# Performance work log

Measured on AMD Instinct MI355X. Metric: run time of the kernel, lower is better.

## Reference

```python
import jax, jax.numpy as jnp
import numpy as np

D_MODEL = 128
N_HEADS = 8
N_POINTS = 8
MAX_RES = 10.0


def setup_inputs() -> dict:
    key = jax.random.key(0)
    ks = jax.random.split(key, 12)
    B, C, H, W = 4, D_MODEL, 128, 128
    nh, P = N_HEADS, N_POINTS
    inp = {
        'nbr_fea': jax.random.normal(ks[0], (B, C, H, W), jnp.float32),
        'ext_fea': jax.random.normal(ks[1], (B, C, H, W), jnp.float32),
        'flow': jax.random.normal(ks[2], (B, 2, H, W), jnp.float32) * 2.0,
        'W_off': jax.random.normal(ks[3], (C, nh * P * 2), jnp.float32) * 0.02,
        'b_off': jax.random.normal(ks[4], (nh * P * 2,), jnp.float32) * 0.02,
        'W_attn': jax.random.normal(ks[5], (C, nh * P), jnp.float32) * 0.02,
        'b_attn': jnp.zeros((nh * P,), jnp.float32),
        'W_val': jax.random.normal(ks[6], (C, C), jnp.float32) * (1.0 / np.sqrt(C)),
        'b_val': jnp.zeros((C,), jnp.float32),
        'W_out': jax.random.normal(ks[7], (C, C), jnp.float32) * (1.0 / np.sqrt(C)),
        'b_out': jnp.zeros((C,), jnp.float32),
    }
    return inp


def _bilinear_gather(value, loc, H, W):
    # value: (B, nh, HW, dh)  loc: (B, nh, Q, P, 2) normalized to [0,1]
    # grid_sample semantics: align_corners=False, zero padding
    B, nh, HW, dh = value.shape
    Q, P = loc.shape[2], loc.shape[3]
    x = loc[..., 0] * W - 0.5  # (B,nh,Q,P) pixel coords
    y = loc[..., 1] * H - 0.5
    x0 = jnp.floor(x)
    y0 = jnp.floor(y)
    wx = x - x0
    wy = y - y0
    out = jnp.zeros((B, nh, Q * P, dh), value.dtype)
    for dx, dy, wgt in ((0, 0, (1 - wx) * (1 - wy)), (1, 0, wx * (1 - wy)),
                        (0, 1, (1 - wx) * wy), (1, 1, wx * wy)):
        xi = x0 + dx
        yi = y0 + dy
        valid = (xi >= 0) & (xi < W) & (yi >= 0) & (yi < H)
        xi_c = jnp.clip(xi, 0, W - 1).astype(jnp.int32)
        yi_c = jnp.clip(yi, 0, H - 1).astype(jnp.int32)
        idx = (yi_c * W + xi_c).reshape(B, nh, Q * P, 1)
        g = jnp.take_along_axis(value, idx, axis=2)  # (B,nh,QP,dh)
        w_eff = (wgt * valid.astype(value.dtype)).reshape(B, nh, Q * P, 1)
        out = out + g * w_eff
    return out.reshape(B, nh, Q, P, dh)


def reference(nbr_fea, ext_fea, flow, W_off, b_off, W_attn, b_attn, W_val, b_val, W_out, b_out):
    B, C, H, W = nbr_fea.shape
    nh, P = N_HEADS, N_POINTS
    dh = C // nh
    Q = H * W
    # normalized reference points (pixel centers / extent)
    ys = (jnp.arange(H, dtype=jnp.float32) + 0.5) / H
    xs = (jnp.arange(W, dtype=jnp.float32) + 0.5) / W
    yy, xx = jnp.meshgrid(ys, xs, indexing='ij')
    ref = jnp.stack([xx, yy], -1).reshape(Q, 2)  # (Q,2)

    ext = ext_fea.transpose(0, 2, 3, 1).reshape(B, Q, C)
    # flow-guided sampling offsets (pixels), residue bounded by tanh
    off = MAX_RES * jnp.tanh(ext @ W_off + b_off)
    off = off.reshape(B, Q, nh, P, 2)
    flow_q = flow.transpose(0, 2, 3, 1).reshape(B, Q, 1, 1, 2)
    norm = jnp.array([W, H], jnp.float32)
    loc = ref[None, :, None, None, :] + (flow_q + off) / norm  # (B,Q,nh,P,2)

    attn = jax.nn.softmax((ext @ W_attn + b_attn).reshape(B, Q, nh, P), axis=-1)

    val = (nbr_fea.transpose(0, 2, 3, 1).reshape(B, Q, C) @ W_val + b_val)
    val = val.reshape(B, Q, nh, dh).transpose(0, 2, 1, 3)  # (B,nh,HW,dh)

    sampled = _bilinear_gather(val, loc.transpose(0, 2, 1, 3, 4), H, W)  # (B,nh,Q,P,dh)
    agg = jnp.einsum('bnqpd,bqnp->bqnd', sampled, attn).reshape(B, Q, C)
    out = agg @ W_out + b_out  # (B,Q,C)
    return out.reshape(B, H, W, C).transpose(0, 3, 1, 2)
```

## Files before the change

### kernel.cpp

```cpp
#include <hip/hip_runtime.h>
#include <math.h>

namespace {
constexpr int B   = 4;
constexpr int C   = 128;
constexpr int H   = 128;
constexpr int W   = 128;
constexpr int HWn = H * W;
constexpr int NH  = 8;
}

using short8 = __attribute__((ext_vector_type(8))) short;
using f32x4  = __attribute__((ext_vector_type(4))) float;

__device__ __forceinline__ float fast_tanh(float x) {
  float e = __expf(2.f * x);
  return 1.f - 2.f / (e + 1.f);
}
__device__ __forceinline__ unsigned f2bf(float f) {
  unsigned u = __float_as_uint(f);
  return (u + 0x7FFFu + ((u >> 16) & 1u)) >> 16;
}
__device__ __forceinline__ unsigned pack2bf(float a, float b) {
  return f2bf(a) | (f2bf(b) << 16);
}

__global__ __launch_bounds__(256) void prep_weights_kernel(
    const float* __restrict__ Woff, const float* __restrict__ Wattn,
    const float* __restrict__ Wval, const float* __restrict__ Wout,
    unsigned short* __restrict__ wcat_t, unsigned short* __restrict__ wval_t,
    unsigned short* __restrict__ wout_t) {
  int row = blockIdx.x * 256 + threadIdx.x;
  if (row >= 448) return;
  const float* src; int ldn; int col; unsigned short* dst;
  if (row < 192) {
    if (row < 128) { src = Woff; ldn = 128; col = row; }
    else           { src = Wattn; ldn = 64; col = row - 128; }
    dst = wcat_t + row * 128;
  } else if (row < 320) {
    src = Wval; ldn = 128; col = row - 192; dst = wval_t + (row - 192) * 128;
  } else {
    src = Wout; ldn = 128; col = row - 320; dst = wout_t + (row - 320) * 128;
  }
  for (int k0 = 0; k0 < 128; k0 += 8) {
    unsigned pk[4];
#pragma unroll
    for (int j = 0; j < 4; ++j)
      pk[j] = pack2bf(src[(k0 + 2 * j) * ldn + col],
                      src[(k0 + 2 * j + 1) * ldn + col]);
    *(uint4*)(dst + k0) = make_uint4(pk[0], pk[1], pk[2], pk[3]);
  }
}

__global__ __launch_bounds__(256) void gemm_kernel(
    const float* __restrict__ nbr,
    const unsigned short* __restrict__ wval_t,
    const float* __restrict__ bv,
    unsigned short* __restrict__ val) {
  __shared__ unsigned short a_s[32 * 152];
  const int t    = threadIdx.x;
  const int id   = blockIdx.x;
  const int b    = id >> 9;
  const int q0   = (id & 511) * 32;
  const int wv   = t >> 6;
  const int lane = t & 63;
  const int li   = lane & 15, quad = lane >> 4;

  const float* Ab = nbr + (size_t)b * C * HWn + q0;
#pragma unroll
  for (int it = 0; it < 2; ++it) {
    int idx = t + 256 * it;
    int kp  = idx >> 3;
    int q4  = (idx & 7) * 4;
    float4 fa = *(const float4*)(Ab + (size_t)(2 * kp) * HWn + q4);
    float4 fb = *(const float4*)(Ab + (size_t)(2 * kp + 1) * HWn + q4);
    const float* pa = &fa.x; const float* pb = &fb.x;
#pragma unroll
    for (int j = 0; j < 4; ++j)
      *(unsigned*)&a_s[(q4 + j) * 152 + 2 * kp] = pack2bf(pa[j], pb[j]);
  }
  __syncthreads();

  const int mt = wv & 1;
  const int ng = (wv >> 1) * 4;
  f32x4 acc[4];
#pragma unroll
  for (int i = 0; i < 4; ++i) acc[i] = (f32x4){0.f, 0.f, 0.f, 0.f};

#pragma unroll 1
  for (int ck = 0; ck < 4; ++ck) {
    short8 af = *(const short8*)&a_s[(16 * mt + li) * 152 + ck * 32 + quad * 8];
#pragma unroll
    for (int i = 0; i < 4; ++i) {
      short8 bfr = *(const short8*)(wval_t + (size_t)(16 * (ng + i) + li) * 128 +
                                    ck * 32 + quad * 8);
      acc[i] = __builtin_amdgcn_mfma_f32_16x16x32_bf16(af, bfr, acc[i], 0, 0, 0);
    }
  }
  __syncthreads();

#pragma unroll
  for (int i = 0; i < 4; ++i) {
    int c = 16 * (ng + i) + li;
    float bias = bv[c];
#pragma unroll
    for (int reg = 0; reg < 4; ++reg) {
      int q = mt * 16 + quad * 4 + reg;
      a_s[q * 152 + c] = (unsigned short)f2bf(acc[i][reg] + bias);
    }
  }
  __syncthreads();

  {
    const int qi = t & 31, hs = t >> 5;
    uint4 v0 = *(const uint4*)&a_s[qi * 152 + 16 * hs];
    uint4 v1 = *(const uint4*)&a_s[qi * 152 + 16 * hs + 8];
    unsigned short* d = val + ((size_t)(b * NH + hs) * HWn + q0 + qi) * 16;
    *(uint4*)d = v0; *(uint4*)(d + 8) = v1;
  }
}

__global__ __launch_bounds__(256) void gather_out_kernel(
    const float* __restrict__ flow, const float* __restrict__ ext,
    const unsigned short* __restrict__ wcat_t,
    const float* __restrict__ boff, const float* __restrict__ battn,
    const unsigned short* __restrict__ val,
    const unsigned short* __restrict__ wout_t, const float* __restrict__ bout,
    float* __restrict__ out) {
  __shared__ float smem[16 * 204];
  unsigned short* a_ext = (unsigned short*)smem;
  float* l_s = smem;
  unsigned short* a_s2 = (unsigned short*)smem;
  float* c_s = smem;

  const int t   = threadIdx.x;
  const int qi  = t & 15;
  const int r   = (t >> 4) & 7;
  const int chh = t >> 7;

  const int blk  = blockIdx.x;
  const int lin  = (blk & 7) * 512 + (blk >> 3);
  const int b    = lin >> 10;
  const int tile = lin & 1023;
  const int x0   = (tile & 7) * 16;
  const int y    = tile >> 3;
  const int x    = x0 + qi;

  const int lane = t & 63;
  const int li   = lane & 15, quad = lane >> 4;
  const int wv   = t >> 6;

  {
    const float* Eb = ext + (size_t)b * C * HWn + (size_t)y * W + x0;
    int kp = t >> 2;
    int xo = (t & 3) * 4;
    float4 fa = *(const float4*)(Eb + (size_t)(2 * kp) * HWn + xo);
    float4 fb = *(const float4*)(Eb + (size_t)(2 * kp + 1) * HWn + xo);
    const float* pa = &fa.x; const float* pb = &fb.x;
#pragma unroll
    for (int j = 0; j < 4; ++j)
      *(unsigned*)&a_ext[(xo + j) * 136 + 2 * kp] = pack2bf(pa[j], pb[j]);
  }
  __syncthreads();

  {
    f32x4 lacc[3];
#pragma unroll
    for (int i = 0; i < 3; ++i) lacc[i] = (f32x4){0.f, 0.f, 0.f, 0.f};

#pragma unroll 1
    for (int ks = 0; ks < 4; ++ks) {
      short8 af = *(const short8*)&a_ext[li * 136 + ks * 32 + quad * 8];
#pragma unroll
      for (int i = 0; i < 3; ++i) {
        int n = wv * 3 + i;
        short8 bfr = *(const short8*)(wcat_t + (size_t)(16 * n + li) * 128 +
                                      ks * 32 + quad * 8);
        lacc[i] = __builtin_amdgcn_mfma_f32_16x16x32_bf16(af, bfr, lacc[i], 0, 0, 0);
      }
    }
    __syncthreads();

#pragma unroll
    for (int i = 0; i < 3; ++i) {
      int col = 16 * (wv * 3 + i) + li;
      float bias = (col < 128) ? boff[col] : battn[col - 128];
#pragma unroll
      for (int reg = 0; reg < 4; ++reg) {
        int q = quad * 4 + reg;
        l_s[q * 204 + col] = lacc[i][reg] + bias;
      }
    }
  }
  __syncthreads();

  const float* lrow = l_s + qi * 204;
  float offa[16];
  float atta[8];
#pragma unroll
  for (int j4 = 0; j4 < 4; ++j4) {
    float4 v = *(const float4*)(lrow + 16 * r + 4 * j4);
    offa[4 * j4 + 0] = 10.f * fast_tanh(v.x);
    offa[4 * j4 + 1] = 10.f * fast_tanh(v.y);
    offa[4 * j4 + 2] = 10.f * fast_tanh(v.z);
    offa[4 * j4 + 3] = 10.f * fast_tanh(v.w);
  }
#pragma unroll
  for (int j4 = 0; j4 < 2; ++j4) {
    float4 v = *(const float4*)(lrow + 128 + 8 * r + 4 * j4);
    atta[4 * j4 + 0] = v.x; atta[4 * j4 + 1] = v.y;
    atta[4 * j4 + 2] = v.z; atta[4 * j4 + 3] = v.w;
  }
  {
    float m = atta[0];
#pragma unroll
    for (int p = 1; p < 8; ++p) m = fmaxf(m, atta[p]);
    float s = 0.f;
#pragma unroll
    for (int p = 0; p < 8; ++p) { float ev = __expf(atta[p] - m); atta[p] = ev; s += ev; }
    float inv = 1.f / s;
#pragma unroll
    for (int p = 0; p < 8; ++p) atta[p] *= inv;
  }
  __syncthreads();

  const float xb = (float)x + flow[(size_t)b * 2 * HWn + y * W + x];
  const float yb = (float)y + flow[((size_t)b * 2 + 1) * HWn + y * W + x];

  float agg[8];
#pragma unroll
  for (int j = 0; j < 8; ++j) agg[j] = 0.f;
  const unsigned short* valh =
      val + ((size_t)b * NH + r) * HWn * 16 + 8 * chh;

#pragma unroll
  for (int p = 0; p < 8; ++p) {
    float sx = xb + offa[2 * p];
    float sy = yb + offa[2 * p + 1];
    float x0f = floorf(sx), y0f = floorf(sy);
    float wx = sx - x0f, wy = sy - y0f;
    int ix0 = (int)x0f, iy0 = (int)y0f;
    int ix1 = ix0 + 1,  iy1 = iy0 + 1;
    float aw  = atta[p];
    float w00 = aw * (1.f - wx) * (1.f - wy);
    float w10 = aw * wx * (1.f - wy);
    float w01 = aw * (1.f - wx) * wy;
    float w11 = aw * wx * wy;
    if ((unsigned)ix0 >= (unsigned)W) { w00 = 0.f; w01 = 0.f; }
    if ((unsigned)ix1 >= (unsigned)W) { w10 = 0.f; w11 = 0.f; }
    if ((unsigned)iy0 >= (unsigned)H) { w00 = 0.f; w10 = 0.f; }
    if ((unsigned)iy1 >= (unsigned)H) { w01 = 0.f; w11 = 0.f; }
    int x0c = min(max(ix0, 0), W - 1);
    int x1c = min(max(ix1, 0), W - 1);
    int y0c = min(max(iy0, 0), H - 1);
    int y1c = min(max(iy1, 0), H - 1);
    const unsigned short* c00 = valh + (size_t)(y0c * W + x0c) * 16;
    const unsigned short* c10 = valh + (size_t)(y0c * W + x1c) * 16;
    const unsigned short* c01 = valh + (size_t)(y1c * W + x0c) * 16;
    const unsigned short* c11 = valh + (size_t)(y1c * W + x1c) * 16;
#pragma unroll
    for (int cn = 0; cn < 4; ++cn) {
      const unsigned short* cp = (cn == 0) ? c00 : (cn == 1) ? c10
                                : (cn == 2) ? c01 : c11;
      float wgt = (cn == 0) ? w00 : (cn == 1) ? w10 : (cn == 2) ? w01 : w11;
      uint4 ga = *(const uint4*)cp;
      unsigned gs[4] = {ga.x, ga.y, ga.z, ga.w};
#pragma unroll
      for (int i = 0; i < 4; ++i) {
        float lo = __uint_as_float(gs[i] << 16);
        float hi = __uint_as_float(gs[i] & 0xFFFF0000u);
        agg[2 * i]     += wgt * lo;
        agg[2 * i + 1] += wgt * hi;
      }
    }
  }

  {
    unsigned pk[4];
#pragma unroll
    for (int j = 0; j < 4; ++j) pk[j] = pack2bf(agg[2 * j], agg[2 * j + 1]);
    *(uint4*)&a_s2[qi * 136 + 16 * r + 8 * chh] =
        make_uint4(pk[0], pk[1], pk[2], pk[3]);
  }
  __syncthreads();

  const int ng = wv * 2;
  f32x4 acc[2];
#pragma unroll
  for (int i = 0; i < 2; ++i) acc[i] = (f32x4){0.f, 0.f, 0.f, 0.f};

#pragma unroll 1
  for (int ks = 0; ks < 4; ++ks) {
    short8 af = *(const short8*)&a_s2[li * 136 + ks * 32 + quad * 8];
#pragma unroll
    for (int i = 0; i < 2; ++i) {
      short8 bfr = *(const short8*)(wout_t + (size_t)(16 * (ng + i) + li) * 128 +
                                    ks * 32 + quad * 8);
      acc[i] = __builtin_amdgcn_mfma_f32_16x16x32_bf16(af, bfr, acc[i], 0, 0, 0);
    }
  }
  __syncthreads();

#pragma unroll
  for (int i = 0; i < 2; ++i) {
    int c = 16 * (ng + i) + li;
    float bias = bout[c];
#pragma unroll
    for (int reg = 0; reg < 4; ++reg) {
      int q = quad * 4 + reg;
      c_s[c * 17 + q] = acc[i][reg] + bias;
    }
  }
  __syncthreads();

  float* ob = out + (size_t)b * C * HWn + (size_t)y * W + x;
#pragma unroll
  for (int j = 0; j < 8; ++j) {
    int cc = 16 * r + 8 * chh + j;
    ob[(size_t)cc * HWn] = c_s[cc * 17 + qi];
  }
}

extern "C" void kernel_launch(void* const* d_in, const int* in_sizes, int n_in,
                              void* d_out, int out_size, void* d_ws, size_t ws_size,
                              hipStream_t stream) {
  const float* nbr   = (const float*)d_in[0];
  const float* extf  = (const float*)d_in[1];
  const float* flow  = (const float*)d_in[2];
  const float* Woff  = (const float*)d_in[3];
  const float* boff  = (const float*)d_in[4];
  const float* Wattn = (const float*)d_in[5];
  const float* battn = (const float*)d_in[6];
  const float* Wval  = (const float*)d_in[7];
  const float* bval  = (const float*)d_in[8];
  const float* Wout  = (const float*)d_in[9];
  const float* bout  = (const float*)d_in[10];
  float* outp = (float*)d_out;

  unsigned short* val    = (unsigned short*)d_ws;
  unsigned short* wcat_t = val + (size_t)B * NH * HWn * 16;
  unsigned short* wval_t = wcat_t + 192 * 128;
  unsigned short* wout_t = wval_t + 128 * 128;

  prep_weights_kernel<<<dim3(2), dim3(256), 0, stream>>>(
      Woff, Wattn, Wval, Wout, wcat_t, wval_t, wout_t);
  gemm_kernel<<<dim3(2048), dim3(256), 0, stream>>>(
      nbr, wval_t, bval, val);
  gather_out_kernel<<<dim3(4096), dim3(256), 0, stream>>>(
      flow, extf, wcat_t, boff, battn, val, wout_t, bout, outp);
}
```

Baseline: 236.0 us.

## Precompute horizontally paired value layout so bilinear taps share one row fetch

Adds a pass that writes each pixel's head values together with its right neighbour's into a doubled-width buffer. The gather kernel then fetches two contiguous 32-byte row pairs instead of four scattered corners, remapping weights when the left tap is out of bounds. This aims to cut the number of scattered memory transactions in the gather. In exchange it adds an extra kernel launch, doubles the value buffer footprint, and adds extra write and read traffic.

Measured after the change: 270.2 us. +14.5%, slower.

```diff
diff --git a/kernel.cpp b/kernel.cpp
--- a/kernel.cpp
+++ b/kernel.cpp
@@ -120,11 +120,27 @@
   }
 }
 
+__global__ __launch_bounds__(256) void pair_kernel(
+    const unsigned short* __restrict__ val,
+    unsigned short* __restrict__ val_pair) {
+  size_t idx = (size_t)blockIdx.x * 256 + threadIdx.x;
+  int x = (int)(idx & (W - 1));
+  const unsigned short* s0 = val + idx * 16;
+  const unsigned short* s1 = s0 + (x < W - 1 ? 16 : 0);
+  uint4 a0 = ((const uint4*)s0)[0];
+  uint4 a1 = ((const uint4*)s0)[1];
+  uint4 b0 = ((const uint4*)s1)[0];
+  uint4 b1 = ((const uint4*)s1)[1];
+  unsigned short* d = val_pair + idx * 32;
+  ((uint4*)d)[0] = a0; ((uint4*)d)[1] = a1;
+  ((uint4*)d)[2] = b0; ((uint4*)d)[3] = b1;
+}
+
 __global__ __launch_bounds__(256) void gather_out_kernel(
     const float* __restrict__ flow, const float* __restrict__ ext,
     const unsigned short* __restrict__ wcat_t,
     const float* __restrict__ boff, const float* __restrict__ battn,
-    const unsigned short* __restrict__ val,
+    const unsigned short* __restrict__ val_pair,
     const unsigned short* __restrict__ wout_t, const float* __restrict__ bout,
     float* __restrict__ out) {
   __shared__ float smem[16 * 204];
@@ -230,8 +246,8 @@
   float agg[8];
 #pragma unroll
   for (int j = 0; j < 8; ++j) agg[j] = 0.f;
-  const unsigned short* valh =
-      val + ((size_t)b * NH + r) * HWn * 16 + 8 * chh;
+  const unsigned short* vph =
+      val_pair + ((size_t)b * NH + r) * HWn * 32 + 8 * chh;
 
 #pragma unroll
   for (int p = 0; p < 8; ++p) {
@@ -250,20 +266,22 @@
     if ((unsigned)ix1 >= (unsigned)W) { w10 = 0.f; w11 = 0.f; }
     if ((unsigned)iy0 >= (unsigned)H) { w00 = 0.f; w10 = 0.f; }
     if ((unsigned)iy1 >= (unsigned)H) { w01 = 0.f; w11 = 0.f; }
-    int x0c = min(max(ix0, 0), W - 1);
-    int x1c = min(max(ix1, 0), W - 1);
+    bool xneg = (ix0 < 0);
+    float wA0 = xneg ? w10 : w00, wB0 = xneg ? 0.f : w10;
+    float wA1 = xneg ? w11 : w01, wB1 = xneg ? 0.f : w11;
+    int bx  = min(max(ix0, 0), W - 1);
     int y0c = min(max(iy0, 0), H - 1);
     int y1c = min(max(iy1, 0), H - 1);
-    const unsigned short* c00 = valh + (size_t)(y0c * W + x0c) * 16;
-    const unsigned short* c10 = valh + (size_t)(y0c * W + x1c) * 16;
-    const unsigned short* c01 = valh + (size_t)(y1c * W + x0c) * 16;
-    const unsigned short* c11 = valh + (size_t)(y1c * W + x1c) * 16;
+    const unsigned short* r0 = vph + (size_t)(y0c * W + bx) * 32;
+    const unsigned short* r1 = vph + (size_t)(y1c * W + bx) * 32;
+    uint4 g00 = *(const uint4*)(r0);
+    uint4 g01 = *(const uint4*)(r0 + 16);
+    uint4 g10 = *(const uint4*)(r1);
+    uint4 g11 = *(const uint4*)(r1 + 16);
 #pragma unroll
     for (int cn = 0; cn < 4; ++cn) {
-      const unsigned short* cp = (cn == 0) ? c00 : (cn == 1) ? c10
-                                : (cn == 2) ? c01 : c11;
-      float wgt = (cn == 0) ? w00 : (cn == 1) ? w10 : (cn == 2) ? w01 : w11;
-      uint4 ga = *(const uint4*)cp;
+      uint4 ga = (cn == 0) ? g00 : (cn == 1) ? g01 : (cn == 2) ? g10 : g11;
+      float wgt = (cn == 0) ? wA0 : (cn == 1) ? wB0 : (cn == 2) ? wA1 : wB1;
       unsigned gs[4] = {ga.x, ga.y, ga.z, ga.w};
 #pragma unroll
       for (int i = 0; i < 4; ++i) {
@@ -337,15 +355,17 @@
   const float* bout  = (const float*)d_in[10];
   float* outp = (float*)d_out;
 
-  unsigned short* val    = (unsigned short*)d_ws;
-  unsigned short* wcat_t = val + (size_t)B * NH * HWn * 16;
-  unsigned short* wval_t = wcat_t + 192 * 128;
-  unsigned short* wout_t = wval_t + 128 * 128;
+  unsigned short* val      = (unsigned short*)d_ws;
+  unsigned short* val_pair = val + (size_t)B * NH * HWn * 16;
+  unsigned short* wcat_t   = val_pair + (size_t)B * NH * HWn * 32;
+  unsigned short* wval_t   = wcat_t + 192 * 128;
+  unsigned short* wout_t   = wval_t + 128 * 128;
 
   prep_weights_kernel<<<dim3(2), dim3(256), 0, stream>>>(
       Woff, Wattn, Wval, Wout, wcat_t, wval_t, wout_t);
   gemm_kernel<<<dim3(2048), dim3(256), 0, stream>>>(
       nbr, wval_t, bval, val);
+  pair_kernel<<<dim3(2048), dim3(256), 0, stream>>>(val, val_pair);
   gather_out_kernel<<<dim3(4096), dim3(256), 0, stream>>>(
-      flow, extf, wcat_t, boff, battn, val, wout_t, bout, outp);
-}
+      flow, extf, wcat_t, boff, battn, val_pair, wout_t, bout, outp);
+}
```
